# Optimization experiments

Hardware: AMD Instinct MI355X
Metric: run time of the kernel (lower is better)

The kernel has to match this reference:

```python
import jax, jax.numpy as jnp
import numpy as np

N = 100000
E = 1600000
IN, HID, OUT = 128, 128, 64


def sage_conv(x, edge_index, W_l, W_r, b):
    # PyG SAGEConv with mean aggregation:
    # out = mean_{j in N(i)} x_j @ W_l + x_i @ W_r + b
    src, dst = edge_index[0], edge_index[1]
    msgs = x[src]                                            # [E, D] gather
    summed = jax.ops.segment_sum(msgs, dst, num_segments=N)  # [N, D] scatter-add
    deg = jax.ops.segment_sum(jnp.ones((E,), x.dtype), dst, num_segments=N)
    mean = summed / jnp.maximum(deg, 1.0)[:, None]
    return mean @ W_l + x @ W_r + b


def setup_inputs() -> dict:
    key = jax.random.key(0)
    ks = jax.random.split(key, 8)
    x = jax.random.normal(ks[0], (N, IN), dtype=jnp.float32)
    edge_index = jax.random.randint(ks[1], (2, E), 0, N, dtype=jnp.int64)
    s1 = 1.0 / np.sqrt(IN)
    s2 = 1.0 / np.sqrt(HID)
    W1_l = jax.random.uniform(ks[2], (IN, HID), jnp.float32, -s1, s1)
    W1_r = jax.random.uniform(ks[3], (IN, HID), jnp.float32, -s1, s1)
    b1 = jnp.zeros((HID,), jnp.float32)
    W2_l = jax.random.uniform(ks[4], (HID, OUT), jnp.float32, -s2, s2)
    W2_r = jax.random.uniform(ks[5], (HID, OUT), jnp.float32, -s2, s2)
    b2 = jnp.zeros((OUT,), jnp.float32)
    return {"x": x, "edge_index": edge_index, "W1_l": W1_l, "W1_r": W1_r,
            "b1": b1, "W2_l": W2_l, "W2_r": W2_r, "b2": b2}


def reference(x, edge_index, W1_l, W1_r, b1, W2_l, W2_r, b2):
    h = sage_conv(x, edge_index, W1_l, W1_r, b1)
    h = jax.nn.relu(h)
    out = sage_conv(h, edge_index, W2_l, W2_r, b2)
    return out
```

## Files before the change

kernel.cpp:

```cpp
#include <hip/hip_runtime.h>

#define NN 100000
#define NE 1600000
#define KB 782
#define BSH 7
#define MAXB 4096
#define PBLK 200

#define OFF_CC    0
#define OFF_RST   1024
#define OFF_RDG   101120
#define OFF_STAGE 201216
#define OFF_XB    3404288
#define OFF_XF8   9810432
#define OFF_MEANB 13013504
#define OFF_W1LP  25825792
#define OFF_W1RP  (25825792 + 8192)
#define OFF_W2LP  (25825792 + 16384)
#define OFF_W2RP  (25825792 + 20480)

typedef __bf16 bf16x8 __attribute__((ext_vector_type(8)));
typedef float f32x4 __attribute__((ext_vector_type(4)));
typedef float f32x2 __attribute__((ext_vector_type(2)));

static __device__ __forceinline__ ushort f2bf(float f) {
    unsigned u = __float_as_uint(f);
    return (ushort)((u + 0x7fffu + ((u >> 16) & 1u)) >> 16);
}
static __device__ __forceinline__ float bflo(unsigned u) { return __uint_as_float(u << 16); }
static __device__ __forceinline__ float bfhi(unsigned u) { return __uint_as_float(u & 0xffff0000u); }

#define PREP_CPART 200
#define PREP_PACKB 6
#define PREP_CVT   3125
#define PREP_GRID  (PREP_CPART + PREP_PACKB + PREP_CVT)

__global__ __launch_bounds__(1024) void prep_kernel(
    const float* __restrict__ x, ushort* __restrict__ xb, unsigned* __restrict__ xf8,
    const float* __restrict__ W1l, const float* __restrict__ W1r,
    const float* __restrict__ W2l, const float* __restrict__ W2r,
    ushort* __restrict__ w1lp, ushort* __restrict__ w1rp,
    ushort* __restrict__ w2lp, ushort* __restrict__ w2rp,
    const int* __restrict__ src, const int* __restrict__ dst,
    int* __restrict__ cc, unsigned* __restrict__ stage) {
    __shared__ int hist[KB];
    __shared__ int cur[KB];
    int bid = blockIdx.x;
    int t = threadIdx.x;

    if (bid >= PREP_CPART + PREP_PACKB) {
        int i = (bid - PREP_CPART - PREP_PACKB) * 1024 + t;
        float4 v = ((const float4*)x)[i];
        uint2 o;
        o.x = (unsigned)f2bf(v.x) | ((unsigned)f2bf(v.y) << 16);
        o.y = (unsigned)f2bf(v.z) | ((unsigned)f2bf(v.w) << 16);
        ((uint2*)xb)[i] = o;
        int p8 = __builtin_amdgcn_cvt_pk_fp8_f32(v.x, v.y, 0, false);
        p8 = __builtin_amdgcn_cvt_pk_fp8_f32(v.z, v.w, p8, true);
        xf8[i] = (unsigned)p8;
        return;
    }

    if (bid >= PREP_CPART) {
        int vb = (bid - PREP_CPART) * 4 + (t >> 8);
        int vt = t & 255;
        const float* W;
        ushort* out;
        int N, frag0;
        if (vb < 8)       { W = W1l; out = w1lp; N = 128; frag0 = vb * 4; }
        else if (vb < 16) { W = W1r; out = w1rp; N = 128; frag0 = (vb - 8) * 4; }
        else if (vb < 20) { W = W2l; out = w2lp; N = 64;  frag0 = (vb - 16) * 4; }
        else              { W = W2r; out = w2rp; N = 64;  frag0 = (vb - 20) * 4; }
        int lane = vt & 63;
        int frag = frag0 + (vt >> 6);
        int NT = N >> 4;
        int ktile = frag / NT, ntile = frag - ktile * NT;
        int k = ktile * 32 + (lane >> 4) * 8;
        int n = ntile * 16 + (lane & 15);
        ushort tmp[8];
#pragma unroll
        for (int j = 0; j < 8; ++j) tmp[j] = f2bf(W[(k + j) * N + n]);
        uint4 o;
        o.x = (unsigned)tmp[0] | ((unsigned)tmp[1] << 16);
        o.y = (unsigned)tmp[2] | ((unsigned)tmp[3] << 16);
        o.z = (unsigned)tmp[4] | ((unsigned)tmp[5] << 16);
        o.w = (unsigned)tmp[6] | ((unsigned)tmp[7] << 16);
        *(uint4*)&out[(frag * 64 + lane) * 8] = o;
        return;
    }

    int e0 = bid * (NE / PBLK);
    int e1 = e0 + (NE / PBLK);
    for (int i = t; i < KB; i += 1024) hist[i] = 0;
    __syncthreads();
    for (int e = e0 + t; e < e1; e += 1024)
        atomicAdd(&hist[dst[e] >> BSH], 1);
    __syncthreads();
    for (int i = t; i < KB; i += 1024) {
        int c = hist[i];
        cur[i] = c ? atomicAdd(&cc[i], c) : 0;
    }
    __syncthreads();
    for (int e = e0 + t; e < e1; e += 1024) {
        int d = dst[e];
        int bkt = d >> BSH;
        int p = atomicAdd(&cur[bkt], 1);
        if (p < MAXB)
            stage[bkt * MAXB + p] = ((unsigned)(d & 127) << 17) | (unsigned)src[e];
    }
}

__global__ __launch_bounds__(256) void sort_kernel(unsigned* __restrict__ stage,
                                                   const int* __restrict__ cc,
                                                   int* __restrict__ rstart,
                                                   int* __restrict__ rdeg) {
    __shared__ unsigned ssrc[MAXB];
    __shared__ int sc[128];
    __shared__ int loff[129];
    __shared__ int lcur[128];
    int t = threadIdx.x;
    int b = blockIdx.x;
    unsigned* st = stage + b * MAXB;
    int cnt = min(cc[b], MAXB);

    if (t < 128) lcur[t] = 0;
    __syncthreads();
    for (int i = t; i < cnt; i += 256) atomicAdd(&lcur[st[i] >> 17], 1);
    __syncthreads();
    if (t < 128) sc[t] = lcur[t];
    __syncthreads();
    for (int off = 1; off < 128; off <<= 1) {
        int v = (t < 128 && t >= off) ? sc[t - off] : 0;
        __syncthreads();
        if (t < 128) sc[t] += v;
        __syncthreads();
    }
    if (t < 128) {
        int excl = (t == 0) ? 0 : sc[t - 1];
        loff[t] = excl;
        lcur[t] = excl;
    }
    if (t == 127) loff[128] = sc[127];
    __syncthreads();
    for (int i = t; i < cnt; i += 256) {
        unsigned v = st[i];
        int p = atomicAdd(&lcur[v >> 17], 1);
        ssrc[p] = v & 0x1FFFFu;
    }
    __syncthreads();
    for (int i = t; i < cnt; i += 256) st[i] = ssrc[i];
    int node0 = b << BSH;
    if (t < 128 && node0 + t < NN) {
        rstart[node0 + t] = b * MAXB + loff[t];
        rdeg[node0 + t] = loff[t + 1] - loff[t];
    }
}

static __device__ __forceinline__ void accum8(float* a, uint2 u) {
    f32x2 p0 = __builtin_amdgcn_cvt_pk_f32_fp8(u.x, false);
    f32x2 p1 = __builtin_amdgcn_cvt_pk_f32_fp8(u.x, true);
    f32x2 p2 = __builtin_amdgcn_cvt_pk_f32_fp8(u.y, false);
    f32x2 p3 = __builtin_amdgcn_cvt_pk_f32_fp8(u.y, true);
    a[0] += p0.x; a[1] += p0.y; a[2] += p1.x; a[3] += p1.y;
    a[4] += p2.x; a[5] += p2.y; a[6] += p3.x; a[7] += p3.y;
}

static __device__ __forceinline__ void writeRow8(ushort* __restrict__ meanb, int node,
                                                 int l4, const float* a, int deg) {
    float inv = 1.0f / fmaxf((float)deg, 1.0f);
    uint4 o;
    o.x = (unsigned)f2bf(a[0] * inv) | ((unsigned)f2bf(a[1] * inv) << 16);
    o.y = (unsigned)f2bf(a[2] * inv) | ((unsigned)f2bf(a[3] * inv) << 16);
    o.z = (unsigned)f2bf(a[4] * inv) | ((unsigned)f2bf(a[5] * inv) << 16);
    o.w = (unsigned)f2bf(a[6] * inv) | ((unsigned)f2bf(a[7] * inv) << 16);
    *(uint4*)&meanb[node * 128 + 8 * l4] = o;
}

__global__ __launch_bounds__(256) void agg1g_kernel(const unsigned* __restrict__ es,
                                                    const int* __restrict__ rstart,
                                                    const int* __restrict__ rdeg,
                                                    const unsigned* __restrict__ xf8,
                                                    ushort* __restrict__ meanb) {
    int t = threadIdx.x;
    int l4 = t & 15;
    int nA = blockIdx.x * 32 + (t >> 4) * 2;
    int nB = nA + 1;
    int sA = rstart[nA], dA = rdeg[nA];
    int sB = rstart[nB], dB = rdeg[nB];
    const uint2* xv = (const uint2*)xf8;
    float aA[8] = {0.f, 0.f, 0.f, 0.f, 0.f, 0.f, 0.f, 0.f};
    float aB[8] = {0.f, 0.f, 0.f, 0.f, 0.f, 0.f, 0.f, 0.f};
    int eA = 0, eB = 0;
    while (eA + 4 <= dA && eB + 4 <= dB) {
        int qa0 = es[sA + eA + 0], qa1 = es[sA + eA + 1];
        int qa2 = es[sA + eA + 2], qa3 = es[sA + eA + 3];
        int qb0 = es[sB + eB + 0], qb1 = es[sB + eB + 1];
        int qb2 = es[sB + eB + 2], qb3 = es[sB + eB + 3];
        uint2 ua0 = xv[qa0 * 16 + l4], ua1 = xv[qa1 * 16 + l4];
        uint2 ua2 = xv[qa2 * 16 + l4], ua3 = xv[qa3 * 16 + l4];
        uint2 ub0 = xv[qb0 * 16 + l4], ub1 = xv[qb1 * 16 + l4];
        uint2 ub2 = xv[qb2 * 16 + l4], ub3 = xv[qb3 * 16 + l4];
        accum8(aA, ua0); accum8(aA, ua1); accum8(aA, ua2); accum8(aA, ua3);
        accum8(aB, ub0); accum8(aB, ub1); accum8(aB, ub2); accum8(aB, ub3);
        eA += 4; eB += 4;
    }
    for (; eA + 4 <= dA; eA += 4) {
        int q0 = es[sA + eA + 0], q1 = es[sA + eA + 1];
        int q2 = es[sA + eA + 2], q3 = es[sA + eA + 3];
        uint2 u0 = xv[q0 * 16 + l4], u1 = xv[q1 * 16 + l4];
        uint2 u2 = xv[q2 * 16 + l4], u3 = xv[q3 * 16 + l4];
        accum8(aA, u0); accum8(aA, u1); accum8(aA, u2); accum8(aA, u3);
    }
    for (; eA < dA; ++eA) accum8(aA, xv[es[sA + eA] * 16 + l4]);
    for (; eB + 4 <= dB; eB += 4) {
        int q0 = es[sB + eB + 0], q1 = es[sB + eB + 1];
        int q2 = es[sB + eB + 2], q3 = es[sB + eB + 3];
        uint2 u0 = xv[q0 * 16 + l4], u1 = xv[q1 * 16 + l4];
        uint2 u2 = xv[q2 * 16 + l4], u3 = xv[q3 * 16 + l4];
        accum8(aB, u0); accum8(aB, u1); accum8(aB, u2); accum8(aB, u3);
    }
    for (; eB < dB; ++eB) accum8(aB, xv[es[sB + eB] * 16 + l4]);

    writeRow8(meanb, nA, l4, aA, dA);
    writeRow8(meanb, nB, l4, aB, dB);
}

__global__ __launch_bounds__(256) void agg2g_kernel(const unsigned* __restrict__ es,
                                                    const int* __restrict__ rstart,
                                                    const int* __restrict__ rdeg,
                                                    const ushort* __restrict__ pb,
                                                    float* __restrict__ out) {
    int t = threadIdx.x;
    int l5 = t & 31;
    int nA = blockIdx.x * 16 + (t >> 5) * 2;
    int nB = nA + 1;
    int sA = rstart[nA], dA = rdeg[nA];
    int sB = rstart[nB], dB = rdeg[nB];
    float2 pA = *(const float2*)&out[(size_t)nA * 64 + 2 * l5];
    float2 pB = *(const float2*)&out[(size_t)nB * 64 + 2 * l5];
    const unsigned* pbu = (const unsigned*)pb;
    float a0 = 0.f, a1 = 0.f, b0 = 0.f, b1 = 0.f;
    int eA = 0, eB = 0;
    while (eA + 4 <= dA && eB + 4 <= dB) {
        int qa0 = es[sA + eA + 0], qa1 = es[sA + eA + 1];
        int qa2 = es[sA + eA + 2], qa3 = es[sA + eA + 3];
        int qb0 = es[sB + eB + 0], qb1 = es[sB + eB + 1];
        int qb2 = es[sB + eB + 2], qb3 = es[sB + eB + 3];
        unsigned ua0 = pbu[qa0 * 32 + l5], ua1 = pbu[qa1 * 32 + l5];
        unsigned ua2 = pbu[qa2 * 32 + l5], ua3 = pbu[qa3 * 32 + l5];
        unsigned ub0 = pbu[qb0 * 32 + l5], ub1 = pbu[qb1 * 32 + l5];
        unsigned ub2 = pbu[qb2 * 32 + l5], ub3 = pbu[qb3 * 32 + l5];
        a0 += bflo(ua0) + bflo(ua1) + bflo(ua2) + bflo(ua3);
        a1 += bfhi(ua0) + bfhi(ua1) + bfhi(ua2) + bfhi(ua3);
        b0 += bflo(ub0) + bflo(ub1) + bflo(ub2) + bflo(ub3);
        b1 += bfhi(ub0) + bfhi(ub1) + bfhi(ub2) + bfhi(ub3);
        eA += 4; eB += 4;
    }
    for (; eA + 4 <= dA; eA += 4) {
        int q0 = es[sA + eA + 0], q1 = es[sA + eA + 1];
        int q2 = es[sA + eA + 2], q3 = es[sA + eA + 3];
        unsigned u0 = pbu[q0 * 32 + l5], u1 = pbu[q1 * 32 + l5];
        unsigned u2 = pbu[q2 * 32 + l5], u3 = pbu[q3 * 32 + l5];
        a0 += bflo(u0) + bflo(u1) + bflo(u2) + bflo(u3);
        a1 += bfhi(u0) + bfhi(u1) + bfhi(u2) + bfhi(u3);
    }
    for (; eA < dA; ++eA) {
        unsigned u = pbu[es[sA + eA] * 32 + l5];
        a0 += bflo(u); a1 += bfhi(u);
    }
    for (; eB + 4 <= dB; eB += 4) {
        int q0 = es[sB + eB + 0], q1 = es[sB + eB + 1];
        int q2 = es[sB + eB + 2], q3 = es[sB + eB + 3];
        unsigned u0 = pbu[q0 * 32 + l5], u1 = pbu[q1 * 32 + l5];
        unsigned u2 = pbu[q2 * 32 + l5], u3 = pbu[q3 * 32 + l5];
        b0 += bflo(u0) + bflo(u1) + bflo(u2) + bflo(u3);
        b1 += bfhi(u0) + bfhi(u1) + bfhi(u2) + bfhi(u3);
    }
    for (; eB < dB; ++eB) {
        unsigned u = pbu[es[sB + eB] * 32 + l5];
        b0 += bflo(u); b1 += bfhi(u);
    }
    float invA = 1.0f / fmaxf((float)dA, 1.0f);
    float invB = 1.0f / fmaxf((float)dB, 1.0f);
    float2 oA = {pA.x + a0 * invA, pA.y + a1 * invA};
    float2 oB = {pB.x + b0 * invB, pB.y + b1 * invB};
    *(float2*)&out[(size_t)nA * 64 + 2 * l5] = oA;
    *(float2*)&out[(size_t)nB * 64 + 2 * l5] = oB;
}

__global__ __launch_bounds__(256) void gemm1_kernel(const ushort* __restrict__ meanb,
                                                    const ushort* __restrict__ xb,
                                                    const ushort* __restrict__ w1lp,
                                                    const ushort* __restrict__ w1rp,
                                                    const float* __restrict__ b1,
                                                    const ushort* __restrict__ w2lp,
                                                    const ushort* __restrict__ w2rp,
                                                    const float* __restrict__ b2,
                                                    ushort* __restrict__ pb,
                                                    float* __restrict__ out) {
    __shared__ ushort As[64 * 136];
    int t = threadIdx.x;
    int node0 = blockIdx.x * 64;
    int w = t >> 6, l = t & 63;
    int lrow = w * 16 + (l & 15);
    int lkq = (l >> 4) * 8;
    int cq = l & 15, rq = (l >> 4) * 4;

    f32x4 acc[8];
#pragma unroll
    for (int i = 0; i < 8; ++i) acc[i] = (f32x4){0.f, 0.f, 0.f, 0.f};

    {
        const uint4* g = (const uint4*)(meanb + (size_t)node0 * 128);
#pragma unroll
        for (int i = 0; i < 4; ++i) {
            int chunk = t + 256 * i;
            *(uint4*)&As[(chunk >> 4) * 136 + (chunk & 15) * 8] = g[chunk];
        }
    }
    __syncthreads();
#pragma unroll
    for (int kt = 0; kt < 4; ++kt) {
        bf16x8 a = *(const bf16x8*)&As[lrow * 136 + kt * 32 + lkq];
        const bf16x8* bp = (const bf16x8*)w1lp + (kt * 8) * 64 + l;
#pragma unroll
        for (int nt = 0; nt < 8; ++nt)
            acc[nt] = __builtin_amdgcn_mfma_f32_16x16x32_bf16(a, bp[nt * 64], acc[nt], 0, 0, 0);
    }
    __syncthreads();

    {
        const uint4* g = (const uint4*)(xb + (size_t)node0 * 128);
#pragma unroll
        for (int i = 0; i < 4; ++i) {
            int chunk = t + 256 * i;
            *(uint4*)&As[(chunk >> 4) * 136 + (chunk & 15) * 8] = g[chunk];
        }
    }
    __syncthreads();
#pragma unroll
    for (int kt = 0; kt < 4; ++kt) {
        bf16x8 a = *(const bf16x8*)&As[lrow * 136 + kt * 32 + lkq];
        const bf16x8* bp = (const bf16x8*)w1rp + (kt * 8) * 64 + l;
#pragma unroll
        for (int nt = 0; nt < 8; ++nt)
            acc[nt] = __builtin_amdgcn_mfma_f32_16x16x32_bf16(a, bp[nt * 64], acc[nt], 0, 0, 0);
    }
    __syncthreads();

#pragma unroll
    for (int nt = 0; nt < 8; ++nt) {
        int n = nt * 16 + cq;
        float bias = b1[n];
#pragma unroll
        for (int r = 0; r < 4; ++r) {
            float hv = fmaxf(acc[nt][r] + bias, 0.0f);
            As[(w * 16 + rq + r) * 136 + n] = f2bf(hv);
        }
    }
    __syncthreads();

    f32x4 acc2[4];
    f32x4 acc3[4];
#pragma unroll
    for (int i = 0; i < 4; ++i) {
        acc2[i] = (f32x4){0.f, 0.f, 0.f, 0.f};
        acc3[i] = (f32x4){0.f, 0.f, 0.f, 0.f};
    }
#pragma unroll
    for (int kt = 0; kt < 4; ++kt) {
        bf16x8 a = *(const bf16x8*)&As[lrow * 136 + kt * 32 + lkq];
        const bf16x8* bpl = (const bf16x8*)w2lp + (kt * 4) * 64 + l;
        const bf16x8* bpr = (const bf16x8*)w2rp + (kt * 4) * 64 + l;
#pragma unroll
        for (int nt = 0; nt < 4; ++nt) {
            acc2[nt] = __builtin_amdgcn_mfma_f32_16x16x32_bf16(a, bpl[nt * 64], acc2[nt], 0, 0, 0);
            acc3[nt] = __builtin_amdgcn_mfma_f32_16x16x32_bf16(a, bpr[nt * 64], acc3[nt], 0, 0, 0);
        }
    }

#pragma unroll
    for (int nt = 0; nt < 4; ++nt) {
        int n = nt * 16 + cq;
        float bias = b2[n];
#pragma unroll
        for (int r = 0; r < 4; ++r) {
            int row = node0 + w * 16 + rq + r;
            if (row < NN)
                out[(size_t)row * 64 + n] = acc3[nt][r] + bias;
        }
    }

    __syncthreads();
#pragma unroll
    for (int nt = 0; nt < 4; ++nt)
#pragma unroll
        for (int r = 0; r < 4; ++r)
            As[(w * 16 + rq + r) * 136 + nt * 16 + cq] = f2bf(acc2[nt][r]);
    __syncthreads();
    {
        uint4* g = (uint4*)(pb + (size_t)node0 * 64);
#pragma unroll
        for (int i = 0; i < 2; ++i) {
            int chunk = t + 256 * i;
            if (node0 + (chunk >> 3) < NN)
                g[chunk] = *(const uint4*)&As[(chunk >> 3) * 136 + (chunk & 7) * 8];
        }
    }
}

extern "C" void kernel_launch(void* const* d_in, const int* in_sizes, int n_in,
                              void* d_out, int out_size, void* d_ws, size_t ws_size,
                              hipStream_t stream) {
    const float* x   = (const float*)d_in[0];
    const int*   ei  = (const int*)d_in[1];
    const float* W1l = (const float*)d_in[2];
    const float* W1r = (const float*)d_in[3];
    const float* b1  = (const float*)d_in[4];
    const float* W2l = (const float*)d_in[5];
    const float* W2r = (const float*)d_in[6];
    const float* b2  = (const float*)d_in[7];

    const int* src = ei;
    const int* dst = ei + NE;

    int*      ws_i   = (int*)d_ws;
    int*      cc     = ws_i + OFF_CC;
    int*      rstart = ws_i + OFF_RST;
    int*      rdeg   = ws_i + OFF_RDG;
    unsigned* stage  = (unsigned*)(ws_i + OFF_STAGE);
    ushort*   xb     = (ushort*)(ws_i + OFF_XB);
    unsigned* xf8    = (unsigned*)(ws_i + OFF_XF8);
    ushort*   pb     = (ushort*)(ws_i + OFF_XF8);
    ushort*   meanb  = (ushort*)(ws_i + OFF_MEANB);
    ushort*   w1lp   = (ushort*)(ws_i + OFF_W1LP);
    ushort*   w1rp   = (ushort*)(ws_i + OFF_W1RP);
    ushort*   w2lp   = (ushort*)(ws_i + OFF_W2LP);
    ushort*   w2rp   = (ushort*)(ws_i + OFF_W2RP);

    hipMemsetAsync(cc, 0, 1024 * sizeof(int), stream);

    prep_kernel<<<PREP_GRID, 1024, 0, stream>>>(
        x, xb, xf8, W1l, W1r, W2l, W2r, w1lp, w1rp, w2lp, w2rp, src, dst, cc, stage);
    sort_kernel<<<KB, 256, 0, stream>>>(stage, cc, rstart, rdeg);

    agg1g_kernel<<<NN / 32, 256, 0, stream>>>(stage, rstart, rdeg, xf8, meanb);
    gemm1_kernel<<<(NN + 63) / 64, 256, 0, stream>>>(meanb, xb, w1lp, w1rp, b1,
                                                     w2lp, w2rp, b2, pb, (float*)d_out);

    agg2g_kernel<<<NN / 16, 256, 0, stream>>>(stage, rstart, rdeg, pb, (float*)d_out);
}
```

Baseline: 251.4 us.

## Split aggregation by feature slice and stage edge indices in LDS

Both aggregation kernels now give each block 64 destination nodes and one of four feature slices. The block first copies that node range's sorted edge indices into shared memory with nontemporal loads, then each group of 4 threads gathers its slice per edge. The aim is to shrink each block's gather footprint for better cache locality and to take index loads off the dependent global-load chain. In exchange, each edge index is read by four blocks instead of one, a block-wide sync is added, and more blocks are launched.

```diff
diff --git a/kernel.cpp b/kernel.cpp
--- a/kernel.cpp
+++ b/kernel.cpp
@@ -156,6 +156,10 @@
     }
 }
 
+#define AGG_NPB  64
+#define AGG_NGRP ((NN + AGG_NPB - 1) / AGG_NPB)
+#define AGG_GRID (AGG_NGRP * 4)
+
 static __device__ __forceinline__ void accum8(float* a, uint2 u) {
     f32x2 p0 = __builtin_amdgcn_cvt_pk_f32_fp8(u.x, false);
     f32x2 p1 = __builtin_amdgcn_cvt_pk_f32_fp8(u.x, true);
@@ -165,127 +169,102 @@
     a[4] += p2.x; a[5] += p2.y; a[6] += p3.x; a[7] += p3.y;
 }
 
-static __device__ __forceinline__ void writeRow8(ushort* __restrict__ meanb, int node,
-                                                 int l4, const float* a, int deg) {
-    float inv = 1.0f / fmaxf((float)deg, 1.0f);
-    uint4 o;
-    o.x = (unsigned)f2bf(a[0] * inv) | ((unsigned)f2bf(a[1] * inv) << 16);
-    o.y = (unsigned)f2bf(a[2] * inv) | ((unsigned)f2bf(a[3] * inv) << 16);
-    o.z = (unsigned)f2bf(a[4] * inv) | ((unsigned)f2bf(a[5] * inv) << 16);
-    o.w = (unsigned)f2bf(a[6] * inv) | ((unsigned)f2bf(a[7] * inv) << 16);
-    *(uint4*)&meanb[node * 128 + 8 * l4] = o;
-}
-
-__global__ __launch_bounds__(256) void agg1g_kernel(const unsigned* __restrict__ es,
+__global__ __launch_bounds__(256) void agg1s_kernel(const unsigned* __restrict__ es,
                                                     const int* __restrict__ rstart,
                                                     const int* __restrict__ rdeg,
                                                     const unsigned* __restrict__ xf8,
                                                     ushort* __restrict__ meanb) {
+    __shared__ unsigned eidx[MAXB];
     int t = threadIdx.x;
-    int l4 = t & 15;
-    int nA = blockIdx.x * 32 + (t >> 4) * 2;
-    int nB = nA + 1;
-    int sA = rstart[nA], dA = rdeg[nA];
-    int sB = rstart[nB], dB = rdeg[nB];
+    int s = blockIdx.x & 3;
+    int node0 = (blockIdx.x >> 2) * AGG_NPB;
+    int nodeL = min(node0 + AGG_NPB - 1, NN - 1);
+    int eBase = rstart[node0];
+    int cnt = rstart[nodeL] + rdeg[nodeL] - eBase;
+    for (int i = t; i < cnt; i += 256)
+        eidx[i] = __builtin_nontemporal_load(&es[eBase + i]);
+    __syncthreads();
+
+    int node = node0 + (t >> 2);
+    int l2 = t & 3;
+    int s0 = 0, deg = 0;
+    if (node < NN) { s0 = rstart[node] - eBase; deg = rdeg[node]; }
     const uint2* xv = (const uint2*)xf8;
-    float aA[8] = {0.f, 0.f, 0.f, 0.f, 0.f, 0.f, 0.f, 0.f};
-    float aB[8] = {0.f, 0.f, 0.f, 0.f, 0.f, 0.f, 0.f, 0.f};
-    int eA = 0, eB = 0;
-    while (eA + 4 <= dA && eB + 4 <= dB) {
-        int qa0 = es[sA + eA + 0], qa1 = es[sA + eA + 1];
-        int qa2 = es[sA + eA + 2], qa3 = es[sA + eA + 3];
-        int qb0 = es[sB + eB + 0], qb1 = es[sB + eB + 1];
-        int qb2 = es[sB + eB + 2], qb3 = es[sB + eB + 3];
-        uint2 ua0 = xv[qa0 * 16 + l4], ua1 = xv[qa1 * 16 + l4];
-        uint2 ua2 = xv[qa2 * 16 + l4], ua3 = xv[qa3 * 16 + l4];
-        uint2 ub0 = xv[qb0 * 16 + l4], ub1 = xv[qb1 * 16 + l4];
-        uint2 ub2 = xv[qb2 * 16 + l4], ub3 = xv[qb3 * 16 + l4];
-        accum8(aA, ua0); accum8(aA, ua1); accum8(aA, ua2); accum8(aA, ua3);
-        accum8(aB, ub0); accum8(aB, ub1); accum8(aB, ub2); accum8(aB, ub3);
-        eA += 4; eB += 4;
-    }
-    for (; eA + 4 <= dA; eA += 4) {
-        int q0 = es[sA + eA + 0], q1 = es[sA + eA + 1];
-        int q2 = es[sA + eA + 2], q3 = es[sA + eA + 3];
-        uint2 u0 = xv[q0 * 16 + l4], u1 = xv[q1 * 16 + l4];
-        uint2 u2 = xv[q2 * 16 + l4], u3 = xv[q3 * 16 + l4];
-        accum8(aA, u0); accum8(aA, u1); accum8(aA, u2); accum8(aA, u3);
-    }
-    for (; eA < dA; ++eA) accum8(aA, xv[es[sA + eA] * 16 + l4]);
-    for (; eB + 4 <= dB; eB += 4) {
-        int q0 = es[sB + eB + 0], q1 = es[sB + eB + 1];
-        int q2 = es[sB + eB + 2], q3 = es[sB + eB + 3];
-        uint2 u0 = xv[q0 * 16 + l4], u1 = xv[q1 * 16 + l4];
-        uint2 u2 = xv[q2 * 16 + l4], u3 = xv[q3 * 16 + l4];
-        accum8(aB, u0); accum8(aB, u1); accum8(aB, u2); accum8(aB, u3);
-    }
-    for (; eB < dB; ++eB) accum8(aB, xv[es[sB + eB] * 16 + l4]);
-
-    writeRow8(meanb, nA, l4, aA, dA);
-    writeRow8(meanb, nB, l4, aB, dB);
-}
-
-__global__ __launch_bounds__(256) void agg2g_kernel(const unsigned* __restrict__ es,
+    int sb = s * 4 + l2;
+    float a[8] = {0.f, 0.f, 0.f, 0.f, 0.f, 0.f, 0.f, 0.f};
+    int e = 0;
+    for (; e + 4 <= deg; e += 4) {
+        int q0 = eidx[s0 + e + 0], q1 = eidx[s0 + e + 1];
+        int q2 = eidx[s0 + e + 2], q3 = eidx[s0 + e + 3];
+        uint2 u0 = xv[q0 * 16 + sb];
+        uint2 u1 = xv[q1 * 16 + sb];
+        uint2 u2 = xv[q2 * 16 + sb];
+        uint2 u3 = xv[q3 * 16 + sb];
+        accum8(a, u0); accum8(a, u1); accum8(a, u2); accum8(a, u3);
+    }
+    for (; e < deg; ++e) accum8(a, xv[eidx[s0 + e] * 16 + sb]);
+
+    if (node < NN) {
+        float inv = 1.0f / fmaxf((float)deg, 1.0f);
+        uint4 o;
+        o.x = (unsigned)f2bf(a[0] * inv) | ((unsigned)f2bf(a[1] * inv) << 16);
+        o.y = (unsigned)f2bf(a[2] * inv) | ((unsigned)f2bf(a[3] * inv) << 16);
+        o.z = (unsigned)f2bf(a[4] * inv) | ((unsigned)f2bf(a[5] * inv) << 16);
+        o.w = (unsigned)f2bf(a[6] * inv) | ((unsigned)f2bf(a[7] * inv) << 16);
+        *(uint4*)&meanb[(size_t)node * 128 + s * 32 + l2 * 8] = o;
+    }
+}
+
+__global__ __launch_bounds__(256) void agg2s_kernel(const unsigned* __restrict__ es,
                                                     const int* __restrict__ rstart,
                                                     const int* __restrict__ rdeg,
                                                     const ushort* __restrict__ pb,
                                                     float* __restrict__ out) {
+    __shared__ unsigned eidx[MAXB];
     int t = threadIdx.x;
-    int l5 = t & 31;
-    int nA = blockIdx.x * 16 + (t >> 5) * 2;
-    int nB = nA + 1;
-    int sA = rstart[nA], dA = rdeg[nA];
-    int sB = rstart[nB], dB = rdeg[nB];
-    float2 pA = *(const float2*)&out[(size_t)nA * 64 + 2 * l5];
-    float2 pB = *(const float2*)&out[(size_t)nB * 64 + 2 * l5];
-    const unsigned* pbu = (const unsigned*)pb;
-    float a0 = 0.f, a1 = 0.f, b0 = 0.f, b1 = 0.f;
-    int eA = 0, eB = 0;
-    while (eA + 4 <= dA && eB + 4 <= dB) {
-        int qa0 = es[sA + eA + 0], qa1 = es[sA + eA + 1];
-        int qa2 = es[sA + eA + 2], qa3 = es[sA + eA + 3];
-        int qb0 = es[sB + eB + 0], qb1 = es[sB + eB + 1];
-        int qb2 = es[sB + eB + 2], qb3 = es[sB + eB + 3];
-        unsigned ua0 = pbu[qa0 * 32 + l5], ua1 = pbu[qa1 * 32 + l5];
-        unsigned ua2 = pbu[qa2 * 32 + l5], ua3 = pbu[qa3 * 32 + l5];
-        unsigned ub0 = pbu[qb0 * 32 + l5], ub1 = pbu[qb1 * 32 + l5];
-        unsigned ub2 = pbu[qb2 * 32 + l5], ub3 = pbu[qb3 * 32 + l5];
-        a0 += bflo(ua0) + bflo(ua1) + bflo(ua2) + bflo(ua3);
-        a1 += bfhi(ua0) + bfhi(ua1) + bfhi(ua2) + bfhi(ua3);
-        b0 += bflo(ub0) + bflo(ub1) + bflo(ub2) + bflo(ub3);
-        b1 += bfhi(ub0) + bfhi(ub1) + bfhi(ub2) + bfhi(ub3);
-        eA += 4; eB += 4;
-    }
-    for (; eA + 4 <= dA; eA += 4) {
-        int q0 = es[sA + eA + 0], q1 = es[sA + eA + 1];
-        int q2 = es[sA + eA + 2], q3 = es[sA + eA + 3];
-        unsigned u0 = pbu[q0 * 32 + l5], u1 = pbu[q1 * 32 + l5];
-        unsigned u2 = pbu[q2 * 32 + l5], u3 = pbu[q3 * 32 + l5];
-        a0 += bflo(u0) + bflo(u1) + bflo(u2) + bflo(u3);
-        a1 += bfhi(u0) + bfhi(u1) + bfhi(u2) + bfhi(u3);
-    }
-    for (; eA < dA; ++eA) {
-        unsigned u = pbu[es[sA + eA] * 32 + l5];
-        a0 += bflo(u); a1 += bfhi(u);
-    }
-    for (; eB + 4 <= dB; eB += 4) {
-        int q0 = es[sB + eB + 0], q1 = es[sB + eB + 1];
-        int q2 = es[sB + eB + 2], q3 = es[sB + eB + 3];
-        unsigned u0 = pbu[q0 * 32 + l5], u1 = pbu[q1 * 32 + l5];
-        unsigned u2 = pbu[q2 * 32 + l5], u3 = pbu[q3 * 32 + l5];
-        b0 += bflo(u0) + bflo(u1) + bflo(u2) + bflo(u3);
-        b1 += bfhi(u0) + bfhi(u1) + bfhi(u2) + bfhi(u3);
-    }
-    for (; eB < dB; ++eB) {
-        unsigned u = pbu[es[sB + eB] * 32 + l5];
-        b0 += bflo(u); b1 += bfhi(u);
-    }
-    float invA = 1.0f / fmaxf((float)dA, 1.0f);
-    float invB = 1.0f / fmaxf((float)dB, 1.0f);
-    float2 oA = {pA.x + a0 * invA, pA.y + a1 * invA};
-    float2 oB = {pB.x + b0 * invB, pB.y + b1 * invB};
-    *(float2*)&out[(size_t)nA * 64 + 2 * l5] = oA;
-    *(float2*)&out[(size_t)nB * 64 + 2 * l5] = oB;
+    int s = blockIdx.x & 3;
+    int node0 = (blockIdx.x >> 2) * AGG_NPB;
+    int nodeL = min(node0 + AGG_NPB - 1, NN - 1);
+    int eBase = rstart[node0];
+    int cnt = rstart[nodeL] + rdeg[nodeL] - eBase;
+    for (int i = t; i < cnt; i += 256)
+        eidx[i] = __builtin_nontemporal_load(&es[eBase + i]);
+    __syncthreads();
+
+    int node = node0 + (t >> 2);
+    int l2 = t & 3;
+    int s0 = 0, deg = 0;
+    if (node < NN) { s0 = rstart[node] - eBase; deg = rdeg[node]; }
+    f32x4 p = {0.f, 0.f, 0.f, 0.f};
+    size_t obase = (size_t)node * 64 + s * 16 + l2 * 4;
+    if (node < NN) p = *(const f32x4*)&out[obase];
+
+    const uint2* pv = (const uint2*)pb;
+    int sb = s * 4 + l2;
+    float a0 = 0.f, a1 = 0.f, a2 = 0.f, a3 = 0.f;
+    int e = 0;
+    for (; e + 4 <= deg; e += 4) {
+        int q0 = eidx[s0 + e + 0], q1 = eidx[s0 + e + 1];
+        int q2 = eidx[s0 + e + 2], q3 = eidx[s0 + e + 3];
+        uint2 u0 = pv[q0 * 16 + sb];
+        uint2 u1 = pv[q1 * 16 + sb];
+        uint2 u2 = pv[q2 * 16 + sb];
+        uint2 u3 = pv[q3 * 16 + sb];
+        a0 += bflo(u0.x) + bflo(u1.x) + bflo(u2.x) + bflo(u3.x);
+        a1 += bfhi(u0.x) + bfhi(u1.x) + bfhi(u2.x) + bfhi(u3.x);
+        a2 += bflo(u0.y) + bflo(u1.y) + bflo(u2.y) + bflo(u3.y);
+        a3 += bfhi(u0.y) + bfhi(u1.y) + bfhi(u2.y) + bfhi(u3.y);
+    }
+    for (; e < deg; ++e) {
+        uint2 u = pv[eidx[s0 + e] * 16 + sb];
+        a0 += bflo(u.x); a1 += bfhi(u.x);
+        a2 += bflo(u.y); a3 += bfhi(u.y);
+    }
+    if (node < NN) {
+        float inv = 1.0f / fmaxf((float)deg, 1.0f);
+        f32x4 o = {p.x + a0 * inv, p.y + a1 * inv, p.z + a2 * inv, p.w + a3 * inv};
+        *(f32x4*)&out[obase] = o;
+    }
 }
 
 __global__ __launch_bounds__(256) void gemm1_kernel(const ushort* __restrict__ meanb,
@@ -438,15 +417,15 @@
     ushort*   w2lp   = (ushort*)(ws_i + OFF_W2LP);
     ushort*   w2rp   = (ushort*)(ws_i + OFF_W2RP);
 
-    hipMemsetAsync(cc, 0, 1024 * sizeof(int), stream);
+    (void)hipMemsetAsync(cc, 0, 1024 * sizeof(int), stream);
 
     prep_kernel<<<PREP_GRID, 1024, 0, stream>>>(
         x, xb, xf8, W1l, W1r, W2l, W2r, w1lp, w1rp, w2lp, w2rp, src, dst, cc, stage);
     sort_kernel<<<KB, 256, 0, stream>>>(stage, cc, rstart, rdeg);
 
-    agg1g_kernel<<<NN / 32, 256, 0, stream>>>(stage, rstart, rdeg, xf8, meanb);
+    agg1s_kernel<<<AGG_GRID, 256, 0, stream>>>(stage, rstart, rdeg, xf8, meanb);
     gemm1_kernel<<<(NN + 63) / 64, 256, 0, stream>>>(meanb, xb, w1lp, w1rp, b1,
                                                      w2lp, w2rp, b2, pb, (float*)d_out);
 
-    agg2g_kernel<<<NN / 16, 256, 0, stream>>>(stage, rstart, rdeg, pb, (float*)d_out);
-}
+    agg2s_kernel<<<AGG_GRID, 256, 0, stream>>>(stage, rstart, rdeg, pb, (float*)d_out);
+}
```

Result: slower. 357.3 us (+42.1%).

## Compute x@W1_r inside the layer-1 gather kernel via interleaved GEMM blocks

Applied to the files above, without the earlier changes.

Moves the self-term GEMM x@W1_r out of gemm1 into the aggregation kernel. Every other block in the first part of the grid runs an MFMA tile and writes the result as bf16 to a new xr buffer, so the compute-bound GEMM overlaps with the memory-bound gather. gemm1 then loads that precomputed partial and adds it before bias and ReLU. The cost is an extra bf16 write and read of an N×128 intermediate plus one more bf16 rounding of the x@W1_r term.

```diff
diff --git a/kernel.cpp b/kernel.cpp
--- a/kernel.cpp
+++ b/kernel.cpp
@@ -14,6 +14,7 @@
 #define OFF_XB    3404288
 #define OFF_XF8   9810432
 #define OFF_MEANB 13013504
+#define OFF_XR    19419648
 #define OFF_W1LP  25825792
 #define OFF_W1RP  (25825792 + 8192)
 #define OFF_W2LP  (25825792 + 16384)
@@ -29,6 +30,7 @@
 }
 static __device__ __forceinline__ float bflo(unsigned u) { return __uint_as_float(u << 16); }
 static __device__ __forceinline__ float bfhi(unsigned u) { return __uint_as_float(u & 0xffff0000u); }
+static __device__ __forceinline__ float bfu(ushort s) { return __uint_as_float((unsigned)s << 16); }
 
 #define PREP_CPART 200
 #define PREP_PACKB 6
@@ -156,6 +158,10 @@
     }
 }
 
+#define A1_GATHER 3125
+#define A1_GEMM   1563
+#define A1_GRID   (A1_GATHER + A1_GEMM)
+
 static __device__ __forceinline__ void accum8(float* a, uint2 u) {
     f32x2 p0 = __builtin_amdgcn_cvt_pk_f32_fp8(u.x, false);
     f32x2 p1 = __builtin_amdgcn_cvt_pk_f32_fp8(u.x, true);
@@ -176,14 +182,68 @@
     *(uint4*)&meanb[node * 128 + 8 * l4] = o;
 }
 
-__global__ __launch_bounds__(256) void agg1g_kernel(const unsigned* __restrict__ es,
-                                                    const int* __restrict__ rstart,
-                                                    const int* __restrict__ rdeg,
-                                                    const unsigned* __restrict__ xf8,
-                                                    ushort* __restrict__ meanb) {
+__global__ __launch_bounds__(256, 8) void agg1f_kernel(const unsigned* __restrict__ es,
+                                                       const int* __restrict__ rstart,
+                                                       const int* __restrict__ rdeg,
+                                                       const unsigned* __restrict__ xf8,
+                                                       ushort* __restrict__ meanb,
+                                                       const ushort* __restrict__ xb,
+                                                       const ushort* __restrict__ w1rp,
+                                                       ushort* __restrict__ xrb) {
+    __shared__ ushort As[64 * 136];
+    int bid = blockIdx.x;
     int t = threadIdx.x;
+
+    bool isGemm = (bid < 2 * A1_GEMM) && (bid & 1);
+    if (isGemm) {
+        int node0 = (bid >> 1) * 64;
+        int w = t >> 6, l = t & 63;
+        int lrow = w * 16 + (l & 15);
+        int lkq = (l >> 4) * 8;
+        int cq = l & 15, rq = (l >> 4) * 4;
+
+        {
+            const uint4* g = (const uint4*)(xb + (size_t)node0 * 128);
+#pragma unroll
+            for (int i = 0; i < 4; ++i) {
+                int chunk = t + 256 * i;
+                *(uint4*)&As[(chunk >> 4) * 136 + (chunk & 15) * 8] = g[chunk];
+            }
+        }
+        __syncthreads();
+        f32x4 acc[8];
+#pragma unroll
+        for (int i = 0; i < 8; ++i) acc[i] = (f32x4){0.f, 0.f, 0.f, 0.f};
+#pragma unroll
+        for (int kt = 0; kt < 4; ++kt) {
+            bf16x8 a = *(const bf16x8*)&As[lrow * 136 + kt * 32 + lkq];
+            const bf16x8* bp = (const bf16x8*)w1rp + (kt * 8) * 64 + l;
+#pragma unroll
+            for (int nt = 0; nt < 8; ++nt)
+                acc[nt] = __builtin_amdgcn_mfma_f32_16x16x32_bf16(a, bp[nt * 64], acc[nt], 0, 0, 0);
+        }
+        __syncthreads();
+#pragma unroll
+        for (int nt = 0; nt < 8; ++nt)
+#pragma unroll
+            for (int r = 0; r < 4; ++r)
+                As[(w * 16 + rq + r) * 136 + nt * 16 + cq] = f2bf(acc[nt][r]);
+        __syncthreads();
+        {
+            uint4* g = (uint4*)(xrb + (size_t)node0 * 128);
+#pragma unroll
+            for (int i = 0; i < 4; ++i) {
+                int chunk = t + 256 * i;
+                if (node0 + (chunk >> 4) < NN)
+                    g[chunk] = *(const uint4*)&As[(chunk >> 4) * 136 + (chunk & 15) * 8];
+            }
+        }
+        return;
+    }
+
+    int gi = (bid < 2 * A1_GEMM) ? (bid >> 1) : (bid - A1_GEMM);
     int l4 = t & 15;
-    int nA = blockIdx.x * 32 + (t >> 4) * 2;
+    int nA = gi * 32 + (t >> 4) * 2;
     int nB = nA + 1;
     int sA = rstart[nA], dA = rdeg[nA];
     int sB = rstart[nB], dB = rdeg[nB];
@@ -289,9 +349,8 @@
 }
 
 __global__ __launch_bounds__(256) void gemm1_kernel(const ushort* __restrict__ meanb,
-                                                    const ushort* __restrict__ xb,
+                                                    const ushort* __restrict__ xrb,
                                                     const ushort* __restrict__ w1lp,
-                                                    const ushort* __restrict__ w1rp,
                                                     const float* __restrict__ b1,
                                                     const ushort* __restrict__ w2lp,
                                                     const ushort* __restrict__ w2rp,
@@ -330,7 +389,7 @@
     __syncthreads();
 
     {
-        const uint4* g = (const uint4*)(xb + (size_t)node0 * 128);
+        const uint4* g = (const uint4*)(xrb + (size_t)node0 * 128);
 #pragma unroll
         for (int i = 0; i < 4; ++i) {
             int chunk = t + 256 * i;
@@ -338,15 +397,6 @@
         }
     }
     __syncthreads();
-#pragma unroll
-    for (int kt = 0; kt < 4; ++kt) {
-        bf16x8 a = *(const bf16x8*)&As[lrow * 136 + kt * 32 + lkq];
-        const bf16x8* bp = (const bf16x8*)w1rp + (kt * 8) * 64 + l;
-#pragma unroll
-        for (int nt = 0; nt < 8; ++nt)
-            acc[nt] = __builtin_amdgcn_mfma_f32_16x16x32_bf16(a, bp[nt * 64], acc[nt], 0, 0, 0);
-    }
-    __syncthreads();
 
 #pragma unroll
     for (int nt = 0; nt < 8; ++nt) {
@@ -354,8 +404,9 @@
         float bias = b1[n];
 #pragma unroll
         for (int r = 0; r < 4; ++r) {
-            float hv = fmaxf(acc[nt][r] + bias, 0.0f);
-            As[(w * 16 + rq + r) * 136 + n] = f2bf(hv);
+            int cell = (w * 16 + rq + r) * 136 + n;
+            float hv = fmaxf(acc[nt][r] + bfu(As[cell]) + bias, 0.0f);
+            As[cell] = f2bf(hv);
         }
     }
     __syncthreads();
@@ -433,19 +484,21 @@
     unsigned* xf8    = (unsigned*)(ws_i + OFF_XF8);
     ushort*   pb     = (ushort*)(ws_i + OFF_XF8);
     ushort*   meanb  = (ushort*)(ws_i + OFF_MEANB);
+    ushort*   xrb    = (ushort*)(ws_i + OFF_XR);
     ushort*   w1lp   = (ushort*)(ws_i + OFF_W1LP);
     ushort*   w1rp   = (ushort*)(ws_i + OFF_W1RP);
     ushort*   w2lp   = (ushort*)(ws_i + OFF_W2LP);
     ushort*   w2rp   = (ushort*)(ws_i + OFF_W2RP);
 
-    hipMemsetAsync(cc, 0, 1024 * sizeof(int), stream);
+    (void)hipMemsetAsync(cc, 0, 1024 * sizeof(int), stream);
 
     prep_kernel<<<PREP_GRID, 1024, 0, stream>>>(
         x, xb, xf8, W1l, W1r, W2l, W2r, w1lp, w1rp, w2lp, w2rp, src, dst, cc, stage);
     sort_kernel<<<KB, 256, 0, stream>>>(stage, cc, rstart, rdeg);
 
-    agg1g_kernel<<<NN / 32, 256, 0, stream>>>(stage, rstart, rdeg, xf8, meanb);
-    gemm1_kernel<<<(NN + 63) / 64, 256, 0, stream>>>(meanb, xb, w1lp, w1rp, b1,
+    agg1f_kernel<<<A1_GRID, 256, 0, stream>>>(stage, rstart, rdeg, xf8, meanb,
+                                              xb, w1rp, xrb);
+    gemm1_kernel<<<(NN + 63) / 64, 256, 0, stream>>>(meanb, xrb, w1lp, b1,
                                                      w2lp, w2rp, b2, pb, (float*)d_out);
 
     agg2g_kernel<<<NN / 16, 256, 0, stream>>>(stage, rstart, rdeg, pb, (float*)d_out);
```

Measured after the change: 263.8 us. 4.9% more time.

## Split edge partition into its own kernel, fuse sort with feature conversion, stage indices in LDS

Applied to the files above, without the earlier changes.

The edge bucketing now runs in a standalone kernel with twice as many blocks. The per-bucket sort is fused into the same launch as the x conversion and weight packing, so those independent jobs overlap and one launch is saved. Both aggregation kernels now copy their block's contiguous edge-index range into shared memory with nontemporal loads before gathering, which replaces repeated global index loads. The cost is extra LDS per aggregation block, which may lower occupancy, and the sort path now runs in 1024-thread blocks that carry more unused threads.

```diff
diff --git a/kernel.cpp b/kernel.cpp
--- a/kernel.cpp
+++ b/kernel.cpp
@@ -5,7 +5,7 @@
 #define KB 782
 #define BSH 7
 #define MAXB 4096
-#define PBLK 200
+#define PBLK 400
 
 #define OFF_CC    0
 #define OFF_RST   1024
@@ -30,26 +30,56 @@
 static __device__ __forceinline__ float bflo(unsigned u) { return __uint_as_float(u << 16); }
 static __device__ __forceinline__ float bfhi(unsigned u) { return __uint_as_float(u & 0xffff0000u); }
 
-#define PREP_CPART 200
-#define PREP_PACKB 6
-#define PREP_CVT   3125
-#define PREP_GRID  (PREP_CPART + PREP_PACKB + PREP_CVT)
-
-__global__ __launch_bounds__(1024) void prep_kernel(
+__global__ __launch_bounds__(1024) void cpart_kernel(const int* __restrict__ src,
+                                                     const int* __restrict__ dst,
+                                                     int* __restrict__ cc,
+                                                     unsigned* __restrict__ stage) {
+    __shared__ int hist[KB];
+    __shared__ int cur[KB];
+    int t = threadIdx.x;
+    int e0 = blockIdx.x * (NE / PBLK);
+    int e1 = e0 + (NE / PBLK);
+    for (int i = t; i < KB; i += 1024) hist[i] = 0;
+    __syncthreads();
+    for (int e = e0 + t; e < e1; e += 1024)
+        atomicAdd(&hist[dst[e] >> BSH], 1);
+    __syncthreads();
+    for (int i = t; i < KB; i += 1024) {
+        int c = hist[i];
+        cur[i] = c ? atomicAdd(&cc[i], c) : 0;
+    }
+    __syncthreads();
+    for (int e = e0 + t; e < e1; e += 1024) {
+        int d = dst[e];
+        int bkt = d >> BSH;
+        int p = atomicAdd(&cur[bkt], 1);
+        if (p < MAXB)
+            stage[bkt * MAXB + p] = ((unsigned)(d & 127) << 17) | (unsigned)src[e];
+    }
+}
+
+#define F2_SORT  KB
+#define F2_PACKB 6
+#define F2_CVT   3125
+#define F2_GRID  (F2_SORT + F2_PACKB + F2_CVT)
+
+__global__ __launch_bounds__(1024) void fused2_kernel(
+    unsigned* __restrict__ stage, const int* __restrict__ cc,
+    int* __restrict__ rstart, int* __restrict__ rdeg,
     const float* __restrict__ x, ushort* __restrict__ xb, unsigned* __restrict__ xf8,
     const float* __restrict__ W1l, const float* __restrict__ W1r,
     const float* __restrict__ W2l, const float* __restrict__ W2r,
     ushort* __restrict__ w1lp, ushort* __restrict__ w1rp,
-    ushort* __restrict__ w2lp, ushort* __restrict__ w2rp,
-    const int* __restrict__ src, const int* __restrict__ dst,
-    int* __restrict__ cc, unsigned* __restrict__ stage) {
-    __shared__ int hist[KB];
-    __shared__ int cur[KB];
+    ushort* __restrict__ w2lp, ushort* __restrict__ w2rp) {
+    __shared__ unsigned ssrc[MAXB];
+    __shared__ int sc[128];
+    __shared__ int loff[129];
+    __shared__ int lcur[128];
     int bid = blockIdx.x;
     int t = threadIdx.x;
 
-    if (bid >= PREP_CPART + PREP_PACKB) {
-        int i = (bid - PREP_CPART - PREP_PACKB) * 1024 + t;
+    if (bid >= F2_SORT + F2_PACKB) {
+        int i = (bid - F2_SORT - F2_PACKB) * 1024 + t;
         float4 v = ((const float4*)x)[i];
         uint2 o;
         o.x = (unsigned)f2bf(v.x) | ((unsigned)f2bf(v.y) << 16);
@@ -61,8 +91,8 @@
         return;
     }
 
-    if (bid >= PREP_CPART) {
-        int vb = (bid - PREP_CPART) * 4 + (t >> 8);
+    if (bid >= F2_SORT) {
+        int vb = (bid - F2_SORT) * 4 + (t >> 8);
         int vt = t & 255;
         const float* W;
         ushort* out;
@@ -89,43 +119,13 @@
         return;
     }
 
-    int e0 = bid * (NE / PBLK);
-    int e1 = e0 + (NE / PBLK);
-    for (int i = t; i < KB; i += 1024) hist[i] = 0;
-    __syncthreads();
-    for (int e = e0 + t; e < e1; e += 1024)
-        atomicAdd(&hist[dst[e] >> BSH], 1);
-    __syncthreads();
-    for (int i = t; i < KB; i += 1024) {
-        int c = hist[i];
-        cur[i] = c ? atomicAdd(&cc[i], c) : 0;
-    }
-    __syncthreads();
-    for (int e = e0 + t; e < e1; e += 1024) {
-        int d = dst[e];
-        int bkt = d >> BSH;
-        int p = atomicAdd(&cur[bkt], 1);
-        if (p < MAXB)
-            stage[bkt * MAXB + p] = ((unsigned)(d & 127) << 17) | (unsigned)src[e];
-    }
-}
-
-__global__ __launch_bounds__(256) void sort_kernel(unsigned* __restrict__ stage,
-                                                   const int* __restrict__ cc,
-                                                   int* __restrict__ rstart,
-                                                   int* __restrict__ rdeg) {
-    __shared__ unsigned ssrc[MAXB];
-    __shared__ int sc[128];
-    __shared__ int loff[129];
-    __shared__ int lcur[128];
-    int t = threadIdx.x;
-    int b = blockIdx.x;
+    int b = bid;
     unsigned* st = stage + b * MAXB;
     int cnt = min(cc[b], MAXB);
 
     if (t < 128) lcur[t] = 0;
     __syncthreads();
-    for (int i = t; i < cnt; i += 256) atomicAdd(&lcur[st[i] >> 17], 1);
+    for (int i = t; i < cnt; i += 1024) atomicAdd(&lcur[st[i] >> 17], 1);
     __syncthreads();
     if (t < 128) sc[t] = lcur[t];
     __syncthreads();
@@ -142,13 +142,13 @@
     }
     if (t == 127) loff[128] = sc[127];
     __syncthreads();
-    for (int i = t; i < cnt; i += 256) {
+    for (int i = t; i < cnt; i += 1024) {
         unsigned v = st[i];
         int p = atomicAdd(&lcur[v >> 17], 1);
         ssrc[p] = v & 0x1FFFFu;
     }
     __syncthreads();
-    for (int i = t; i < cnt; i += 256) st[i] = ssrc[i];
+    for (int i = t; i < cnt; i += 1024) st[i] = ssrc[i];
     int node0 = b << BSH;
     if (t < 128 && node0 + t < NN) {
         rstart[node0 + t] = b * MAXB + loff[t];
@@ -181,21 +181,30 @@
                                                     const int* __restrict__ rdeg,
                                                     const unsigned* __restrict__ xf8,
                                                     ushort* __restrict__ meanb) {
+    __shared__ unsigned eidx[MAXB];
     int t = threadIdx.x;
+    int node0 = blockIdx.x * 32;
+    int eBase = rstart[node0];
+    int last = node0 + 31;
+    int cnt = rstart[last] + rdeg[last] - eBase;
+    for (int i = t; i < cnt; i += 256)
+        eidx[i] = __builtin_nontemporal_load(&es[eBase + i]);
+    __syncthreads();
+
     int l4 = t & 15;
-    int nA = blockIdx.x * 32 + (t >> 4) * 2;
+    int nA = node0 + (t >> 4) * 2;
     int nB = nA + 1;
-    int sA = rstart[nA], dA = rdeg[nA];
-    int sB = rstart[nB], dB = rdeg[nB];
+    int sA = rstart[nA] - eBase, dA = rdeg[nA];
+    int sB = rstart[nB] - eBase, dB = rdeg[nB];
     const uint2* xv = (const uint2*)xf8;
     float aA[8] = {0.f, 0.f, 0.f, 0.f, 0.f, 0.f, 0.f, 0.f};
     float aB[8] = {0.f, 0.f, 0.f, 0.f, 0.f, 0.f, 0.f, 0.f};
     int eA = 0, eB = 0;
     while (eA + 4 <= dA && eB + 4 <= dB) {
-        int qa0 = es[sA + eA + 0], qa1 = es[sA + eA + 1];
-        int qa2 = es[sA + eA + 2], qa3 = es[sA + eA + 3];
-        int qb0 = es[sB + eB + 0], qb1 = es[sB + eB + 1];
-        int qb2 = es[sB + eB + 2], qb3 = es[sB + eB + 3];
+        int qa0 = eidx[sA + eA + 0], qa1 = eidx[sA + eA + 1];
+        int qa2 = eidx[sA + eA + 2], qa3 = eidx[sA + eA + 3];
+        int qb0 = eidx[sB + eB + 0], qb1 = eidx[sB + eB + 1];
+        int qb2 = eidx[sB + eB + 2], qb3 = eidx[sB + eB + 3];
         uint2 ua0 = xv[qa0 * 16 + l4], ua1 = xv[qa1 * 16 + l4];
         uint2 ua2 = xv[qa2 * 16 + l4], ua3 = xv[qa3 * 16 + l4];
         uint2 ub0 = xv[qb0 * 16 + l4], ub1 = xv[qb1 * 16 + l4];
@@ -205,21 +214,21 @@
         eA += 4; eB += 4;
     }
     for (; eA + 4 <= dA; eA += 4) {
-        int q0 = es[sA + eA + 0], q1 = es[sA + eA + 1];
-        int q2 = es[sA + eA + 2], q3 = es[sA + eA + 3];
+        int q0 = eidx[sA + eA + 0], q1 = eidx[sA + eA + 1];
+        int q2 = eidx[sA + eA + 2], q3 = eidx[sA + eA + 3];
         uint2 u0 = xv[q0 * 16 + l4], u1 = xv[q1 * 16 + l4];
         uint2 u2 = xv[q2 * 16 + l4], u3 = xv[q3 * 16 + l4];
         accum8(aA, u0); accum8(aA, u1); accum8(aA, u2); accum8(aA, u3);
     }
-    for (; eA < dA; ++eA) accum8(aA, xv[es[sA + eA] * 16 + l4]);
+    for (; eA < dA; ++eA) accum8(aA, xv[eidx[sA + eA] * 16 + l4]);
     for (; eB + 4 <= dB; eB += 4) {
-        int q0 = es[sB + eB + 0], q1 = es[sB + eB + 1];
-        int q2 = es[sB + eB + 2], q3 = es[sB + eB + 3];
+        int q0 = eidx[sB + eB + 0], q1 = eidx[sB + eB + 1];
+        int q2 = eidx[sB + eB + 2], q3 = eidx[sB + eB + 3];
         uint2 u0 = xv[q0 * 16 + l4], u1 = xv[q1 * 16 + l4];
         uint2 u2 = xv[q2 * 16 + l4], u3 = xv[q3 * 16 + l4];
         accum8(aB, u0); accum8(aB, u1); accum8(aB, u2); accum8(aB, u3);
     }
-    for (; eB < dB; ++eB) accum8(aB, xv[es[sB + eB] * 16 + l4]);
+    for (; eB < dB; ++eB) accum8(aB, xv[eidx[sB + eB] * 16 + l4]);
 
     writeRow8(meanb, nA, l4, aA, dA);
     writeRow8(meanb, nB, l4, aB, dB);
@@ -230,22 +239,31 @@
                                                     const int* __restrict__ rdeg,
                                                     const ushort* __restrict__ pb,
                                                     float* __restrict__ out) {
+    __shared__ unsigned eidx[MAXB];
     int t = threadIdx.x;
+    int node0 = blockIdx.x * 16;
+    int eBase = rstart[node0];
+    int last = node0 + 15;
+    int cnt = rstart[last] + rdeg[last] - eBase;
+    for (int i = t; i < cnt; i += 256)
+        eidx[i] = __builtin_nontemporal_load(&es[eBase + i]);
+    __syncthreads();
+
     int l5 = t & 31;
-    int nA = blockIdx.x * 16 + (t >> 5) * 2;
+    int nA = node0 + (t >> 5) * 2;
     int nB = nA + 1;
-    int sA = rstart[nA], dA = rdeg[nA];
-    int sB = rstart[nB], dB = rdeg[nB];
+    int sA = rstart[nA] - eBase, dA = rdeg[nA];
+    int sB = rstart[nB] - eBase, dB = rdeg[nB];
     float2 pA = *(const float2*)&out[(size_t)nA * 64 + 2 * l5];
     float2 pB = *(const float2*)&out[(size_t)nB * 64 + 2 * l5];
     const unsigned* pbu = (const unsigned*)pb;
     float a0 = 0.f, a1 = 0.f, b0 = 0.f, b1 = 0.f;
     int eA = 0, eB = 0;
     while (eA + 4 <= dA && eB + 4 <= dB) {
-        int qa0 = es[sA + eA + 0], qa1 = es[sA + eA + 1];
-        int qa2 = es[sA + eA + 2], qa3 = es[sA + eA + 3];
-        int qb0 = es[sB + eB + 0], qb1 = es[sB + eB + 1];
-        int qb2 = es[sB + eB + 2], qb3 = es[sB + eB + 3];
+        int qa0 = eidx[sA + eA + 0], qa1 = eidx[sA + eA + 1];
+        int qa2 = eidx[sA + eA + 2], qa3 = eidx[sA + eA + 3];
+        int qb0 = eidx[sB + eB + 0], qb1 = eidx[sB + eB + 1];
+        int qb2 = eidx[sB + eB + 2], qb3 = eidx[sB + eB + 3];
         unsigned ua0 = pbu[qa0 * 32 + l5], ua1 = pbu[qa1 * 32 + l5];
         unsigned ua2 = pbu[qa2 * 32 + l5], ua3 = pbu[qa3 * 32 + l5];
         unsigned ub0 = pbu[qb0 * 32 + l5], ub1 = pbu[qb1 * 32 + l5];
@@ -257,27 +275,27 @@
         eA += 4; eB += 4;
     }
     for (; eA + 4 <= dA; eA += 4) {
-        int q0 = es[sA + eA + 0], q1 = es[sA + eA + 1];
-        int q2 = es[sA + eA + 2], q3 = es[sA + eA + 3];
+        int q0 = eidx[sA + eA + 0], q1 = eidx[sA + eA + 1];
+        int q2 = eidx[sA + eA + 2], q3 = eidx[sA + eA + 3];
         unsigned u0 = pbu[q0 * 32 + l5], u1 = pbu[q1 * 32 + l5];
         unsigned u2 = pbu[q2 * 32 + l5], u3 = pbu[q3 * 32 + l5];
         a0 += bflo(u0) + bflo(u1) + bflo(u2) + bflo(u3);
         a1 += bfhi(u0) + bfhi(u1) + bfhi(u2) + bfhi(u3);
     }
     for (; eA < dA; ++eA) {
-        unsigned u = pbu[es[sA + eA] * 32 + l5];
+        unsigned u = pbu[eidx[sA + eA] * 32 + l5];
         a0 += bflo(u); a1 += bfhi(u);
     }
     for (; eB + 4 <= dB; eB += 4) {
-        int q0 = es[sB + eB + 0], q1 = es[sB + eB + 1];
-        int q2 = es[sB + eB + 2], q3 = es[sB + eB + 3];
+        int q0 = eidx[sB + eB + 0], q1 = eidx[sB + eB + 1];
+        int q2 = eidx[sB + eB + 2], q3 = eidx[sB + eB + 3];
         unsigned u0 = pbu[q0 * 32 + l5], u1 = pbu[q1 * 32 + l5];
         unsigned u2 = pbu[q2 * 32 + l5], u3 = pbu[q3 * 32 + l5];
         b0 += bflo(u0) + bflo(u1) + bflo(u2) + bflo(u3);
         b1 += bfhi(u0) + bfhi(u1) + bfhi(u2) + bfhi(u3);
     }
     for (; eB < dB; ++eB) {
-        unsigned u = pbu[es[sB + eB] * 32 + l5];
+        unsigned u = pbu[eidx[sB + eB] * 32 + l5];
         b0 += bflo(u); b1 += bfhi(u);
     }
     float invA = 1.0f / fmaxf((float)dA, 1.0f);
@@ -438,11 +456,12 @@
     ushort*   w2lp   = (ushort*)(ws_i + OFF_W2LP);
     ushort*   w2rp   = (ushort*)(ws_i + OFF_W2RP);
 
-    hipMemsetAsync(cc, 0, 1024 * sizeof(int), stream);
-
-    prep_kernel<<<PREP_GRID, 1024, 0, stream>>>(
-        x, xb, xf8, W1l, W1r, W2l, W2r, w1lp, w1rp, w2lp, w2rp, src, dst, cc, stage);
-    sort_kernel<<<KB, 256, 0, stream>>>(stage, cc, rstart, rdeg);
+    (void)hipMemsetAsync(cc, 0, 1024 * sizeof(int), stream);
+
+    cpart_kernel<<<PBLK, 1024, 0, stream>>>(src, dst, cc, stage);
+    fused2_kernel<<<F2_GRID, 1024, 0, stream>>>(
+        stage, cc, rstart, rdeg, x, xb, xf8,
+        W1l, W1r, W2l, W2r, w1lp, w1rp, w2lp, w2rp);
 
     agg1g_kernel<<<NN / 32, 256, 0, stream>>>(stage, rstart, rdeg, xf8, meanb);
     gemm1_kernel<<<(NN + 63) / 64, 256, 0, stream>>>(meanb, xb, w1lp, w1rp, b1,
```

Measured after the change: 245.3 us. 1.02x faster.
